# Optimization experiments

Measured on AMD Instinct MI355X. Metric: run time of the kernel, lower is better.

## Reference

```python
import jax, jax.numpy as jnp
import numpy as np

B, T, D = 2, 2048, 1024
H, DH = 16, 64


def setup_inputs() -> dict:
    key = jax.random.key(0)
    ks = jax.random.split(key, 8)
    return {
        "x": jax.random.normal(ks[0], (B, T, D), dtype=jnp.float32),
        "mask": jnp.ones((1, 1, T, T), dtype=bool),
        "Wq": jax.random.normal(ks[1], (D, D), dtype=jnp.float32) * 0.02,
        "Wk": jax.random.normal(ks[2], (D, D), dtype=jnp.float32) * 0.02,
        "Wv": jax.random.normal(ks[3], (D, D), dtype=jnp.float32) * 0.02,
        "Wo": jax.random.normal(ks[4], (D, D), dtype=jnp.float32) * 0.02,
        "S_q": jax.random.normal(ks[5], (H, DH, DH), dtype=jnp.float32),
        "S_k": jax.random.normal(ks[6], (H, DH, DH), dtype=jnp.float32),
    }


def reference(x, mask, Wq, Wk, Wv, Wo, S_q, S_k):
    b, t, _ = x.shape
    scale = DH ** (-0.5)
    # nn.Linear applies x @ W.T; our Wq etc. are the Linear weight matrices.
    def split_heads(y):
        return y.reshape(b, t, H, DH).transpose(0, 2, 1, 3)  # (B,H,T,DH)

    Q = split_heads(x @ Wq.T)
    K = split_heads(x @ Wk.T)
    V = split_heads(x @ Wv.T)
    Qp = jnp.einsum('bhtd,hde->bhte', Q, S_q)
    Kp = jnp.einsum('bhtd,hde->bhte', K, S_k)
    scores = jnp.einsum('bhte,bhse->bhts', Qp, Kp) * scale  # (B,H,T,T)
    scores = jnp.where(mask, scores, -jnp.inf)
    attn = jax.nn.softmax(scores, axis=-1)
    out = jnp.einsum('bhts,bhsd->bhtd', attn, V)
    out = out.transpose(0, 2, 1, 3).reshape(b, t, D)
    return out @ Wo.T
```

## Files before the change

kernel.cpp:

```cpp
#include <hip/hip_runtime.h>
#include <cstdint>
#include <cmath>


#define B_   2
#define T_   2048
#define Dm   1024
#define H_   16
#define DH_  64
#define Ntok (B_ * T_)
#define ND   (Ntok * Dm)
#define DD   (Dm * Dm)
#define QKS  2048

typedef _Float16 f16;
typedef _Float16 f16x4 __attribute__((ext_vector_type(4)));
typedef _Float16 f16x8 __attribute__((ext_vector_type(8)));
typedef float    f32x4 __attribute__((ext_vector_type(4)));

__device__ inline f32x4 mfma16(f16x8 a, f16x8 b, f32x4 c) {
  return __builtin_amdgcn_mfma_f32_16x16x32_f16(a, b, c, 0, 0, 0);
}

__device__ inline void async16(const void* g, void* l) {
  __builtin_amdgcn_global_load_lds(
      (const __attribute__((address_space(1))) unsigned int*)g,
      (__attribute__((address_space(3))) unsigned int*)l, 16, 0, 0);
}

__global__ void cvt_f16(const float* __restrict__ X, f16* __restrict__ Y, int n) {
  int i = (blockIdx.x * 256 + threadIdx.x) * 4;
  if (i >= n) return;
  f32x4 v = *(const f32x4*)(X + i);
  f16x4 o;
#pragma unroll
  for (int j = 0; j < 4; ++j) o[j] = (f16)v[j];
  *(f16x4*)(Y + i) = o;
}

__global__ __launch_bounds__(64) void fold_w(const float* __restrict__ W,
                                             const float* __restrict__ S,
                                             f16* __restrict__ T) {
  __shared__ __align__(16) float sS[64 * 64];
  const int tid = threadIdx.x;
  const int h = blockIdx.y;
  const int d = blockIdx.x * 64 + tid;
#pragma unroll 8
  for (int i = 0; i < 64; ++i) sS[i * 64 + tid] = S[h * 4096 + i * 64 + tid];
  __syncthreads();
  float acc[64];
#pragma unroll
  for (int e = 0; e < 64; ++e) acc[e] = 0.f;
  for (int c = 0; c < 64; ++c) {
    float wv = W[(size_t)(h * 64 + c) * Dm + d];
    const f32x4* srow = (const f32x4*)&sS[c * 64];
#pragma unroll
    for (int e4 = 0; e4 < 16; ++e4) {
      f32x4 sv = srow[e4];
      acc[e4 * 4 + 0] += wv * sv[0];
      acc[e4 * 4 + 1] += wv * sv[1];
      acc[e4 * 4 + 2] += wv * sv[2];
      acc[e4 * 4 + 3] += wv * sv[3];
    }
  }
#pragma unroll
  for (int e = 0; e < 64; ++e)
    T[(size_t)(h * 64 + e) * Dm + d] = (f16)acc[e];
}

template <int OUTMODE, int TN>
__global__ __launch_bounds__(256) void gemm_bt(
    const f16* __restrict__ A, const f16* __restrict__ B,
    float* __restrict__ Cf, f16* __restrict__ Ch, f16* __restrict__ Ct,
    int M, int N, int K) {
  constexpr int AS = 128 * 32;
  constexpr int BS = TN * 32;
  constexpr int MT = (TN == 128) ? 4 : 2;
  extern __shared__ __align__(16) f16 smem[];
  f16* sA = smem;
  f16* sB = smem + AS;

  const int tid = threadIdx.x;
  const int w = tid >> 6, lane = tid & 63, g = lane >> 4, ln = lane & 15;
  const int wm = (TN == 128) ? (w >> 1) * 64 : w * 32;
  const int wn = (TN == 128) ? (w & 1) * 64 : 0;
  const int bm = blockIdx.y * 128, bn = blockIdx.x * TN;

  f32x4 acc[MT][4] = {};
  const int r0 = tid >> 2;
  const int kb = (tid & 3) * 8;

  for (int kc = 0; kc < K; kc += 32) {
#pragma unroll
    for (int i = 0; i < 2; ++i) {
      size_t aoff = (size_t)(bm + i * 64 + r0) * K + kc + kb;
      int lo = i * 4096 + w * 1024;
      async16(A + aoff, (char*)sA + lo);
      if (TN == 128 || i == 0) {
        size_t boff = (size_t)(bn + i * 64 + r0) * K + kc + kb;
        async16(B + boff, (char*)sB + lo);
      }
    }
    __syncthreads();
    f16x8 af[MT];
#pragma unroll
    for (int mt = 0; mt < MT; ++mt)
      af[mt] = *(f16x8*)&sA[(wm + mt * 16 + ln) * 32 + g * 8];
#pragma unroll
    for (int nt = 0; nt < 4; ++nt) {
      f16x8 bf = *(f16x8*)&sB[(wn + nt * 16 + ln) * 32 + g * 8];
#pragma unroll
      for (int mt = 0; mt < MT; ++mt)
        acc[mt][nt] = mfma16(af[mt], bf, acc[mt][nt]);
    }
    __syncthreads();
  }

  if (OUTMODE == 3 && bn >= 2048) {
#pragma unroll
    for (int mt = 0; mt < MT; ++mt)
#pragma unroll
      for (int nt = 0; nt < 4; ++nt) {
        int ch = bn - 2048 + wn + nt * 16 + ln;
        size_t base = (size_t)ch * Ntok + bm + wm + mt * 16 + g * 4;
        f16x4 ov;
#pragma unroll
        for (int r = 0; r < 4; ++r) ov[r] = (f16)acc[mt][nt][r];
        *(f16x4*)&Ct[base] = ov;
      }
    return;
  }
#pragma unroll
  for (int mt = 0; mt < MT; ++mt)
#pragma unroll
    for (int nt = 0; nt < 4; ++nt)
#pragma unroll
      for (int r = 0; r < 4; ++r) {
        int row = bm + wm + mt * 16 + g * 4 + r;
        int col = bn + wn + nt * 16 + ln;
        float v = acc[mt][nt][r];
        if (OUTMODE == 0) {
          Cf[(size_t)row * N + col] = v;
        } else {
          Ch[(size_t)row * QKS + col] = (f16)v;
        }
      }
}

__global__ __launch_bounds__(512) void flash_attn(
    const f16* __restrict__ QK, const f16* __restrict__ Vt,
    f16* __restrict__ O) {
  __shared__ __align__(16) f16 sK[64 * 64];
  __shared__ __align__(16) f16 sVT[64 * 64];
  __shared__ __align__(16) f16 sP[8 * 16 * 88];

  const int tid = threadIdx.x;
  const int w = tid >> 6, lane = tid & 63, g = lane >> 4, ln = lane & 15;
  const int bh = blockIdx.y, b = bh >> 4, h = bh & 15;
  const int q0 = blockIdx.x * 128 + w * 16;
  const size_t rowBase = (size_t)b * T_;
  const int hc = h * DH_;

  f16x8 qf[2];
  {
    size_t qrow = (rowBase + q0 + ln) * (size_t)QKS + hc;
#pragma unroll
    for (int s = 0; s < 2; ++s)
      qf[s] = *(const f16x8*)(QK + qrow + s * 32 + g * 8);
  }

  float mrow = -INFINITY, lrow = 0.f;
  f32x4 oacc[4] = {};

  const int srow = tid >> 3;
  const int sel = ((tid & 7) * 8) ^ ((srow & 7) * 8);
  const int ldsoff = tid * 16;

  for (int kc = 0; kc < T_; kc += 64) {
    {
      size_t koff = (rowBase + kc + srow) * (size_t)QKS + 1024 + hc + sel;
      async16(QK + koff, (char*)sK + ldsoff);
      size_t voff = (size_t)(hc + srow) * Ntok + rowBase + kc + sel;
      async16(Vt + voff, (char*)sVT + ldsoff);
    }
    __syncthreads();

    f32x4 s4[4];
#pragma unroll
    for (int nt = 0; nt < 4; ++nt) {
      f32x4 a = {};
#pragma unroll
      for (int s = 0; s < 2; ++s) {
        int col = (s * 32 + g * 8) ^ ((ln & 7) * 8);
        f16x8 k8 = *(const f16x8*)&sK[(nt * 16 + ln) * 64 + col];
        a = mfma16(k8, qf[s], a);
      }
      s4[nt] = a * 0.1803368801111244f;
    }

    float mx = s4[0][0];
#pragma unroll
    for (int nt = 0; nt < 4; ++nt)
#pragma unroll
      for (int r = 0; r < 4; ++r) mx = fmaxf(mx, s4[nt][r]);
    mx = fmaxf(mx, __shfl_xor(mx, 16, 64));
    mx = fmaxf(mx, __shfl_xor(mx, 32, 64));
    float mn = fmaxf(mrow, mx);
    float alpha = __builtin_amdgcn_exp2f(mrow - mn);
    mrow = mn;
    float sum = 0.f;
    f16x4 pk[4];
#pragma unroll
    for (int nt = 0; nt < 4; ++nt)
#pragma unroll
      for (int r = 0; r < 4; ++r) {
        float pv = __builtin_amdgcn_exp2f(s4[nt][r] - mn);
        sum += pv;
        pk[nt][r] = (f16)pv;
      }
    sum += __shfl_xor(sum, 16, 64);
    sum += __shfl_xor(sum, 32, 64);
    lrow = lrow * alpha + sum;
#pragma unroll
    for (int dt = 0; dt < 4; ++dt) oacc[dt] *= alpha;

    f16* pw = sP + w * (16 * 88);
#pragma unroll
    for (int nt = 0; nt < 4; ++nt)
      *(f16x4*)&pw[ln * 88 + nt * 16 + g * 4] = pk[nt];

    asm volatile("" ::: "memory");

#pragma unroll
    for (int s = 0; s < 2; ++s) {
      f16x8 pb = *(const f16x8*)&pw[ln * 88 + s * 32 + g * 8];
#pragma unroll
      for (int dt = 0; dt < 4; ++dt) {
        int col = (s * 32 + g * 8) ^ ((ln & 7) * 8);
        f16x8 va = *(const f16x8*)&sVT[(dt * 16 + ln) * 64 + col];
        oacc[dt] = mfma16(va, pb, oacc[dt]);
      }
    }
    __syncthreads();
  }

  float rl = 1.0f / lrow;
  size_t orow = (rowBase + q0 + ln) * (size_t)Dm + hc;
#pragma unroll
  for (int dt = 0; dt < 4; ++dt) {
    f16x4 ov;
#pragma unroll
    for (int r = 0; r < 4; ++r) ov[r] = (f16)(oacc[dt][r] * rl);
    *(f16x4*)&O[orow + dt * 16 + g * 4] = ov;
  }
}

extern "C" void kernel_launch(void* const* d_in, const int* in_sizes, int n_in,
                              void* d_out, int out_size, void* d_ws, size_t ws_size,
                              hipStream_t stream) {
  const float* x  = (const float*)d_in[0];
  const float* Wq = (const float*)d_in[2];
  const float* Wk = (const float*)d_in[3];
  const float* Wv = (const float*)d_in[4];
  const float* Wo = (const float*)d_in[5];
  const float* Sq = (const float*)d_in[6];
  const float* Sk = (const float*)d_in[7];

  char* p = (char*)d_ws;
  auto alloc = [&](size_t bytes) {
    char* r = p;
    p += (bytes + 255) & ~(size_t)255;
    return r;
  };
  f16* x_f   = (f16*)alloc((size_t)ND * 2);
  f16* Wqkv  = (f16*)alloc((size_t)3 * DD * 2);
  f16* Wo_f  = (f16*)alloc((size_t)DD * 2);
  f16* QK    = (f16*)alloc((size_t)Ntok * QKS * 2);
  f16* Vt_f  = (f16*)alloc((size_t)ND * 2);
  f16* AO    = (f16*)alloc((size_t)ND * 2);

  cvt_f16<<<ND / 1024, 256, 0, stream>>>(x, x_f, ND);
  cvt_f16<<<DD / 1024, 256, 0, stream>>>(Wv, Wqkv + (size_t)2048 * Dm, DD);
  cvt_f16<<<DD / 1024, 256, 0, stream>>>(Wo, Wo_f, DD);
  fold_w<<<dim3(16, 16), 64, 0, stream>>>(Wq, Sq, Wqkv);
  fold_w<<<dim3(16, 16), 64, 0, stream>>>(Wk, Sk, Wqkv + (size_t)1024 * Dm);

  gemm_bt<3, 128><<<dim3(3072 / 128, Ntok / 128), 256, 16384, stream>>>(
      x_f, Wqkv, nullptr, QK, Vt_f, Ntok, 3072, Dm);

  flash_attn<<<dim3(T_ / 128, B_ * H_), 512, 0, stream>>>(QK, Vt_f, AO);

  gemm_bt<0, 64><<<dim3(Dm / 64, Ntok / 128), 256, 12288, stream>>>(
      AO, Wo_f, (float*)d_out, nullptr, nullptr, Ntok, Dm, Dm);
}
```

Baseline: 255.1 us.

## Double-buffer LDS tiles in GEMM and flash attention with one barrier per step

```diff
diff --git a/kernel.cpp b/kernel.cpp
--- a/kernel.cpp
+++ b/kernel.cpp
@@ -26,6 +26,13 @@
   __builtin_amdgcn_global_load_lds(
       (const __attribute__((address_space(1))) unsigned int*)g,
       (__attribute__((address_space(3))) unsigned int*)l, 16, 0, 0);
+}
+
+__device__ inline float vmax4(f32x4 v) {
+  return fmaxf(fmaxf(v[0], v[1]), fmaxf(v[2], v[3]));
+}
+__device__ inline float vsum4(f32x4 v) {
+  return (v[0] + v[1]) + (v[2] + v[3]);
 }
 
 __global__ void cvt_f16(const float* __restrict__ X, f16* __restrict__ Y, int n) {
@@ -77,8 +84,6 @@
   constexpr int BS = TN * 32;
   constexpr int MT = (TN == 128) ? 4 : 2;
   extern __shared__ __align__(16) f16 smem[];
-  f16* sA = smem;
-  f16* sB = smem + AS;
 
   const int tid = threadIdx.x;
   const int w = tid >> 6, lane = tid & 63, g = lane >> 4, ln = lane & 15;
@@ -90,30 +95,39 @@
   const int r0 = tid >> 2;
   const int kb = (tid & 3) * 8;
 
-  for (int kc = 0; kc < K; kc += 32) {
+  auto issue = [&](int kc, int buf) {
+    f16* dA = smem + buf * AS;
+    f16* dB = smem + 2 * AS + buf * BS;
 #pragma unroll
     for (int i = 0; i < 2; ++i) {
       size_t aoff = (size_t)(bm + i * 64 + r0) * K + kc + kb;
       int lo = i * 4096 + w * 1024;
-      async16(A + aoff, (char*)sA + lo);
+      async16(A + aoff, (char*)dA + lo);
       if (TN == 128 || i == 0) {
         size_t boff = (size_t)(bn + i * 64 + r0) * K + kc + kb;
-        async16(B + boff, (char*)sB + lo);
-      }
-    }
+        async16(B + boff, (char*)dB + lo);
+      }
+    }
+  };
+
+  issue(0, 0);
+  const int KI = K / 32;
+  for (int i = 0; i < KI; ++i) {
     __syncthreads();
+    if (i + 1 < KI) issue((i + 1) * 32, (i + 1) & 1);
+    const f16* cA = smem + (i & 1) * AS;
+    const f16* cB = smem + 2 * AS + (i & 1) * BS;
     f16x8 af[MT];
 #pragma unroll
     for (int mt = 0; mt < MT; ++mt)
-      af[mt] = *(f16x8*)&sA[(wm + mt * 16 + ln) * 32 + g * 8];
+      af[mt] = *(const f16x8*)&cA[(wm + mt * 16 + ln) * 32 + g * 8];
 #pragma unroll
     for (int nt = 0; nt < 4; ++nt) {
-      f16x8 bf = *(f16x8*)&sB[(wn + nt * 16 + ln) * 32 + g * 8];
+      f16x8 bf = *(const f16x8*)&cB[(wn + nt * 16 + ln) * 32 + g * 8];
 #pragma unroll
       for (int mt = 0; mt < MT; ++mt)
         acc[mt][nt] = mfma16(af[mt], bf, acc[mt][nt]);
     }
-    __syncthreads();
   }
 
   if (OUTMODE == 3 && bn >= 2048) {
@@ -150,9 +164,9 @@
 __global__ __launch_bounds__(512) void flash_attn(
     const f16* __restrict__ QK, const f16* __restrict__ Vt,
     f16* __restrict__ O) {
-  __shared__ __align__(16) f16 sK[64 * 64];
-  __shared__ __align__(16) f16 sVT[64 * 64];
+  __shared__ __align__(16) f16 sKV[2][2 * 64 * 64];
   __shared__ __align__(16) f16 sP[8 * 16 * 88];
+  constexpr int VOFF = 64 * 64;
 
   const int tid = threadIdx.x;
   const int w = tid >> 6, lane = tid & 63, g = lane >> 4, ln = lane & 15;
@@ -176,14 +190,21 @@
   const int sel = ((tid & 7) * 8) ^ ((srow & 7) * 8);
   const int ldsoff = tid * 16;
 
-  for (int kc = 0; kc < T_; kc += 64) {
-    {
-      size_t koff = (rowBase + kc + srow) * (size_t)QKS + 1024 + hc + sel;
-      async16(QK + koff, (char*)sK + ldsoff);
-      size_t voff = (size_t)(hc + srow) * Ntok + rowBase + kc + sel;
-      async16(Vt + voff, (char*)sVT + ldsoff);
-    }
+  auto issue = [&](int kc, int buf) {
+    f16* base = &sKV[buf][0];
+    size_t koff = (rowBase + kc + srow) * (size_t)QKS + 1024 + hc + sel;
+    async16(QK + koff, (char*)base + ldsoff);
+    size_t voff = (size_t)(hc + srow) * Ntok + rowBase + kc + sel;
+    async16(Vt + voff, (char*)(base + VOFF) + ldsoff);
+  };
+
+  issue(0, 0);
+  constexpr int NC = T_ / 64;
+  for (int i = 0; i < NC; ++i) {
     __syncthreads();
+    if (i + 1 < NC) issue((i + 1) * 64, (i + 1) & 1);
+    const f16* cK = &sKV[i & 1][0];
+    const f16* cVT = cK + VOFF;
 
     f32x4 s4[4];
 #pragma unroll
@@ -192,32 +213,39 @@
 #pragma unroll
       for (int s = 0; s < 2; ++s) {
         int col = (s * 32 + g * 8) ^ ((ln & 7) * 8);
-        f16x8 k8 = *(const f16x8*)&sK[(nt * 16 + ln) * 64 + col];
+        f16x8 k8 = *(const f16x8*)&cK[(nt * 16 + ln) * 64 + col];
         a = mfma16(k8, qf[s], a);
       }
       s4[nt] = a * 0.1803368801111244f;
     }
 
-    float mx = s4[0][0];
-#pragma unroll
-    for (int nt = 0; nt < 4; ++nt)
-#pragma unroll
-      for (int r = 0; r < 4; ++r) mx = fmaxf(mx, s4[nt][r]);
+    f32x4 m4 = s4[0];
+#pragma unroll
+    for (int nt = 1; nt < 4; ++nt) {
+      m4[0] = fmaxf(m4[0], s4[nt][0]);
+      m4[1] = fmaxf(m4[1], s4[nt][1]);
+      m4[2] = fmaxf(m4[2], s4[nt][2]);
+      m4[3] = fmaxf(m4[3], s4[nt][3]);
+    }
+    float mx = vmax4(m4);
     mx = fmaxf(mx, __shfl_xor(mx, 16, 64));
     mx = fmaxf(mx, __shfl_xor(mx, 32, 64));
     float mn = fmaxf(mrow, mx);
     float alpha = __builtin_amdgcn_exp2f(mrow - mn);
     mrow = mn;
-    float sum = 0.f;
+    f32x4 p4[4];
     f16x4 pk[4];
 #pragma unroll
-    for (int nt = 0; nt < 4; ++nt)
+    for (int nt = 0; nt < 4; ++nt) {
 #pragma unroll
       for (int r = 0; r < 4; ++r) {
         float pv = __builtin_amdgcn_exp2f(s4[nt][r] - mn);
-        sum += pv;
+        p4[nt][r] = pv;
         pk[nt][r] = (f16)pv;
       }
+    }
+    f32x4 sv4 = (p4[0] + p4[1]) + (p4[2] + p4[3]);
+    float sum = vsum4(sv4);
     sum += __shfl_xor(sum, 16, 64);
     sum += __shfl_xor(sum, 32, 64);
     lrow = lrow * alpha + sum;
@@ -237,11 +265,10 @@
 #pragma unroll
       for (int dt = 0; dt < 4; ++dt) {
         int col = (s * 32 + g * 8) ^ ((ln & 7) * 8);
-        f16x8 va = *(const f16x8*)&sVT[(dt * 16 + ln) * 64 + col];
+        f16x8 va = *(const f16x8*)&cVT[(dt * 16 + ln) * 64 + col];
         oacc[dt] = mfma16(va, pb, oacc[dt]);
       }
     }
-    __syncthreads();
   }
 
   float rl = 1.0f / lrow;
@@ -285,11 +312,11 @@
   fold_w<<<dim3(16, 16), 64, 0, stream>>>(Wq, Sq, Wqkv);
   fold_w<<<dim3(16, 16), 64, 0, stream>>>(Wk, Sk, Wqkv + (size_t)1024 * Dm);
 
-  gemm_bt<3, 128><<<dim3(3072 / 128, Ntok / 128), 256, 16384, stream>>>(
+  gemm_bt<3, 128><<<dim3(3072 / 128, Ntok / 128), 256, 32768, stream>>>(
       x_f, Wqkv, nullptr, QK, Vt_f, Ntok, 3072, Dm);
 
   flash_attn<<<dim3(T_ / 128, B_ * H_), 512, 0, stream>>>(QK, Vt_f, AO);
 
-  gemm_bt<0, 64><<<dim3(Dm / 64, Ntok / 128), 256, 12288, stream>>>(
+  gemm_bt<0, 64><<<dim3(Dm / 64, Ntok / 128), 256, 24576, stream>>>(
       AO, Wo_f, (float*)d_out, nullptr, nullptr, Ntok, Dm, Dm);
 }
```

Measured after the change: 250.9 us. About the same (-1.7%).
